# Optimization experiments

Hardware: AMD Instinct MI355X
Metric: run time of the kernel (lower is better)

Reference implementation:

```python
import jax, jax.numpy as jnp
import numpy as np

B, T = 64, 1024
RNN_DIM = 256          # lstm input/hidden dim
HID2 = 512             # 2*rnn_hidden_dim (bi-encoder output per char)
POS_DIM = 100
POS_SIZE = 48
LABEL = 96
POS_PAD = 0
APP_ID = 1


def setup_inputs() -> dict:
    key = jax.random.key(0)
    ks = jax.random.split(key, 9)
    s = 0.1
    enc = jax.random.normal(ks[0], (B, T, HID2), jnp.float32)
    pos_id = jax.random.randint(ks[1], (T, B), 0, POS_SIZE)
    start_index = jax.random.randint(ks[2], (T, B), 0, T)
    pos_table = (jax.random.normal(ks[3], (POS_SIZE, POS_DIM), jnp.float32) * s).at[POS_PAD].set(0.0)
    W_ih = jax.random.normal(ks[4], (4 * RNN_DIM, RNN_DIM), jnp.float32) * s
    b_ih = jnp.zeros((4 * RNN_DIM,), jnp.float32)
    W_hh = jax.random.normal(ks[5], (4 * RNN_DIM, RNN_DIM), jnp.float32) * s
    b_hh = jnp.zeros((4 * RNN_DIM,), jnp.float32)
    comb_W = jax.random.normal(ks[6], (RNN_DIM, HID2 + POS_DIM), jnp.float32) * s
    comb_b = jnp.zeros((RNN_DIM,), jnp.float32)
    lin_W = jax.random.normal(ks[7], (LABEL, HID2 + RNN_DIM), jnp.float32) * s
    return {"encoder_out": enc, "pos_table": pos_table, "W_ih": W_ih, "b_ih": b_ih,
            "W_hh": W_hh, "b_hh": b_hh, "comb_W": comb_W, "comb_b": comb_b,
            "lin_W": lin_W, "pos_id": pos_id, "start_index": start_index}


def reference(encoder_out, pos_table, W_ih, b_ih, W_hh, b_hh, comb_W, comb_b, lin_W,
              pos_id, start_index):
    Bn, Tn, D2 = encoder_out.shape
    H = W_hh.shape[1]
    L = lin_W.shape[0]
    dt = encoder_out.dtype
    # prefix sums: P[:, t] = sum of encoder_out[:, :t]  -> [B, T+1, D2]
    P = jnp.concatenate([jnp.zeros((Bn, 1, D2), dt), jnp.cumsum(encoder_out, axis=1)], axis=1)
    # step t consumes decisions made at step t-1 (state.pos_id[-1] / words_startindex[-1])
    prev_pos = jnp.concatenate([jnp.zeros((1, Bn), pos_id.dtype), pos_id[:-1]], axis=0)
    prev_start = jnp.concatenate([jnp.zeros((1, Bn), start_index.dtype), start_index[:-1]], axis=0)
    ts = jnp.arange(Tn)
    enc_t = jnp.swapaxes(encoder_out, 0, 1)   # [T, B, D2]
    P_t = jnp.swapaxes(P[:, :Tn], 0, 1)       # [T, B, D2]; P_t[t] = prefix up to t
    barange = jnp.arange(Bn)
    lab = jnp.arange(L)

    def step(carry, xs):
        h, c = carry
        t, pp, ps, Pt, et = xs
        # variable-length word avg-pool over chars [start, t)  (F.avg_pool1d)
        valid = (ps >= 0) & (t > 0)
        start = jnp.clip(jnp.minimum(ps, t - 1), 0, Tn - 1)
        wsum = Pt - P[barange, start]                       # [B, D2]
        length = jnp.maximum(t - start, 1).astype(dt)
        avg = jnp.where(valid[:, None], wsum / length[:, None], jnp.zeros((), dt))
        pe = pos_table[pp]                                  # [B, pos_dim]
        z = jnp.tanh(jnp.concatenate([pe, avg], axis=1) @ comb_W.T + comb_b)
        z = jnp.where(t > 0, z, jnp.zeros((), dt))          # t==0: z bucket of zeros
        # LSTMCell
        gates = z @ W_ih.T + b_ih + h @ W_hh.T + b_hh
        i_g, f_g, g_g, o_g = jnp.split(gates, 4, axis=1)
        c_new = jax.nn.sigmoid(f_g) * c + jax.nn.sigmoid(i_g) * jnp.tanh(g_g)
        h_new = jax.nn.sigmoid(o_g) * jnp.tanh(c_new)
        # output projection over [h_now, encoder_out[t]]
        out = jnp.concatenate([h_new, et], axis=1) @ lin_W.T
        out = jnp.where((t == 0) & (lab[None, :] == APP_ID), jnp.asarray(-1e10, dt), out)
        return (h_new, c_new), out

    h0 = jnp.zeros((Bn, H), dt)
    (_, _), outs = jax.lax.scan(step, (h0, h0), (ts, prev_pos, prev_start, P_t, enc_t))
    dec = jnp.swapaxes(outs, 0, 1).reshape(Bn * Tn, L)   # cat along dim 1 then view
    return jax.nn.log_softmax(dec, axis=1)
```

## Files before the change

kernel.cpp:

```cpp
#include <hip/hip_runtime.h>

typedef unsigned short u16;
typedef unsigned int u32;
typedef unsigned long long u64;
typedef __attribute__((ext_vector_type(8))) short short8;
typedef __attribute__((ext_vector_type(4))) float f32x4;
typedef __attribute__((ext_vector_type(8))) int i32x8;

#define B_ 64
#define T_ 1024
#define D2_ 512
#define HD_ 256
#define G4_ 1024
#define PD_ 100
#define KX_ 640
#define KO_ 768
#define LBL_ 96
#define LPAD_ 128
#define SCA 125
#define SCB 124

__device__ __forceinline__ float bf2f(u16 u) {
  u32 v = ((u32)u) << 16;
  return __builtin_bit_cast(float, v);
}
__device__ __forceinline__ u16 f2bf(float f) {
  u32 u = __builtin_bit_cast(u32, f);
  u32 r = (u + 0x7fffu + ((u >> 16) & 1u)) >> 16;
  return (u16)r;
}
__device__ __forceinline__ u32 pk2(float a, float b) {
  return (u32)f2bf(a) | ((u32)f2bf(b) << 16);
}
__device__ __forceinline__ float sgm(float x) {
  return __builtin_amdgcn_rcpf(1.f + __builtin_amdgcn_exp2f(-1.442695040888963f * x));
}
__device__ __forceinline__ float thh(float x) {
  return fmaf(-2.f,
              __builtin_amdgcn_rcpf(1.f + __builtin_amdgcn_exp2f(2.885390081777927f * x)),
              1.f);
}
__device__ __forceinline__ u32 enc4(float y) {
  float a = fabsf(y);
  u32 c = 0;
  c = a >= 0.25f ? 1u : c;
  c = a >= 0.75f ? 2u : c;
  c = a >= 1.25f ? 3u : c;
  c = a >= 1.75f ? 4u : c;
  c = a >= 2.5f ? 5u : c;
  c = a >= 3.5f ? 6u : c;
  c = a >= 5.0f ? 7u : c;
  return c | ((__builtin_bit_cast(u32, y) >> 28) & 8u);
}

__global__ __launch_bounds__(256) void k_prep(
    const float* combW, const float* Wih, const float* bih, const float* Whh,
    const float* bhh, const float* linW, u16* wc, u16* wih, u32* w4, u16* wlin,
    float* biasg) {
  int idx = blockIdx.x * 256 + threadIdx.x;
  if (idx < 256 * KX_) {
    int r = idx / KX_, c = idx % KX_;
    wc[idx] = f2bf(c < 612 ? combW[r * 612 + c] : 0.f);
    return;
  }
  idx -= 256 * KX_;
  if (idx < G4_ * HD_) { wih[idx] = f2bf(Wih[idx]); return; }
  idx -= G4_ * HD_;
  if (idx < G4_ * HD_ / 8) {
    int n = idx >> 5, c0 = (idx & 31) * 8;
    const float* wr = Whh + n * 256 + c0;
    u32 word = 0;
#pragma unroll
    for (int i = 0; i < 4; ++i) {
      u32 byte = enc4(wr[2 * i] * 8.f) | (enc4(wr[2 * i + 1] * 8.f) << 4);
      word |= byte << (8 * i);
    }
    w4[n * 32 + (c0 >> 3)] = word;
    return;
  }
  idx -= G4_ * HD_ / 8;
  if (idx < LPAD_ * KO_) {
    int r = idx / KO_;
    wlin[idx] = f2bf(r < LBL_ ? linW[idx] : 0.f);
    return;
  }
  idx -= LPAD_ * KO_;
  if (idx < G4_) biasg[idx] = bih[idx] + bhh[idx];
}

__global__ __launch_bounds__(512) void k_psum(const float* enc, float* S) {
  const int bc = blockIdx.x;
  const int d = threadIdx.x;
  const int b = bc >> 4, c = bc & 15;
  const float* e = enc + (((size_t)b * T_) + c * 64) * D2_ + d;
  float s = 0.f;
#pragma unroll 8
  for (int j = 0; j < 64; ++j) s += e[(size_t)j * D2_];
  S[(size_t)bc * D2_ + d] = s;
}

__global__ __launch_bounds__(512) void k_pwrite(const float* enc, const float* S,
                                                float* P) {
  const int bc = blockIdx.x;
  const int d = threadIdx.x;
  const int b = bc >> 4, c = bc & 15;
  float off = 0.f;
  for (int c2 = 0; c2 < c; ++c2) off += S[((size_t)(b * 16 + c2)) * D2_ + d];
  const float* e = enc + (((size_t)b * T_) + c * 64) * D2_ + d;
  float* p = P + (((size_t)b * T_) + c * 64) * D2_ + d;
#pragma unroll 4
  for (int j = 0; j < 64; ++j) {
    p[(size_t)j * D2_] = off;
    off += e[(size_t)j * D2_];
  }
}

__global__ __launch_bounds__(320) void k_xbuild(const float* P, const float* ptab,
                                                const int* pid, const int* sidx,
                                                u16* X) {
  const int tid = threadIdx.x;
  const int row = tid / 80;
  const int ir = tid - row * 80;
  const int m = blockIdx.x * 4 + row;
  const int t = m >> 6, b = m & 63;
  int pp = 0, ps = 0;
  if (t > 0) {
    pp = pid[(t - 1) * B_ + b];
    ps = sidx[(t - 1) * B_ + b];
  }
  bool valid = (ps >= 0) && (t > 0);
  int start = min(ps, t - 1);
  start = max(start, 0);
  start = min(start, T_ - 1);
  float invlen = 1.f / (float)max(t - start, 1);
  const float* Pt = P + ((size_t)b * T_ + t) * D2_;
  const float* Ps = P + ((size_t)b * T_ + start) * D2_;
  const int k0 = ir * 8;
  uint4 o;
  if (k0 >= 104 && k0 + 8 <= 612) {
    if (valid) {
      int d = k0 - 100;
      float4 t0 = *(const float4*)(Pt + d), t1 = *(const float4*)(Pt + d + 4);
      float4 s0 = *(const float4*)(Ps + d), s1 = *(const float4*)(Ps + d + 4);
      o.x = pk2((t0.x - s0.x) * invlen, (t0.y - s0.y) * invlen);
      o.y = pk2((t0.z - s0.z) * invlen, (t0.w - s0.w) * invlen);
      o.z = pk2((t1.x - s1.x) * invlen, (t1.y - s1.y) * invlen);
      o.w = pk2((t1.z - s1.z) * invlen, (t1.w - s1.w) * invlen);
    } else {
      o = (uint4){0, 0, 0, 0};
    }
  } else if (k0 + 8 <= 100) {
    const float* pr = ptab + pp * PD_ + k0;
    o.x = pk2(pr[0], pr[1]);
    o.y = pk2(pr[2], pr[3]);
    o.z = pk2(pr[4], pr[5]);
    o.w = pk2(pr[6], pr[7]);
  } else if (k0 >= 616) {
    o = (uint4){0, 0, 0, 0};
  } else {
    u32 ow[4];
#pragma unroll
    for (int j2 = 0; j2 < 4; ++j2) {
      float v[2];
#pragma unroll
      for (int jj = 0; jj < 2; ++jj) {
        int k = k0 + j2 * 2 + jj;
        float x;
        if (k < PD_) x = ptab[pp * PD_ + k];
        else if (k < 612) x = valid ? (Pt[k - PD_] - Ps[k - PD_]) * invlen : 0.f;
        else x = 0.f;
        v[jj] = x;
      }
      ow[j2] = pk2(v[0], v[1]);
    }
    o = (uint4){ow[0], ow[1], ow[2], ow[3]};
  }
  *(uint4*)(X + (size_t)m * KX_ + k0) = o;
}

template <int MODE>
__global__ __launch_bounds__(256, 2) void k_gemm(const u16* A, const u16* Bw,
                                                 const float* bias, u16* outb) {
  constexpr int K = (MODE == 0) ? KX_ : HD_;
  constexpr int NOUT = (MODE == 0) ? 256 : 1024;
  __shared__ u16 As[128][40];
  __shared__ u16 Bs[128][40];
  const int m0 = blockIdx.x * 128, n0 = blockIdx.y * 128;
  const int tid = threadIdx.x;
  const int w = tid >> 6, l = tid & 63;
  const int wr = w >> 1, wc = w & 1;
  const int l15 = l & 15, lh = l >> 4;
  const int srow = tid >> 2, sc8 = (tid & 3) * 8;
  int brow0, brow1;
  if constexpr (MODE == 1) {
    int j0 = n0 + srow, j1 = n0 + srow + 64;
    brow0 = (j0 & 3) * 256 + (j0 >> 2);
    brow1 = (j1 & 3) * 256 + (j1 >> 2);
  } else {
    brow0 = n0 + srow;
    brow1 = n0 + srow + 64;
  }
  f32x4 acc[4][4] = {};
  for (int k0 = 0; k0 < K; k0 += 32) {
    uint4 a0 = *(const uint4*)(A + (size_t)(m0 + srow) * K + k0 + sc8);
    uint4 a1 = *(const uint4*)(A + (size_t)(m0 + srow + 64) * K + k0 + sc8);
    uint4 b0 = *(const uint4*)(Bw + (size_t)brow0 * K + k0 + sc8);
    uint4 b1 = *(const uint4*)(Bw + (size_t)brow1 * K + k0 + sc8);
    __syncthreads();
    *(uint4*)&As[srow][sc8] = a0;
    *(uint4*)&As[srow + 64][sc8] = a1;
    *(uint4*)&Bs[srow][sc8] = b0;
    *(uint4*)&Bs[srow + 64][sc8] = b1;
    __syncthreads();
    short8 af[4], bf[4];
#pragma unroll
    for (int i = 0; i < 4; ++i) {
      af[i] = *(const short8*)&As[wr * 64 + i * 16 + l15][lh * 8];
      bf[i] = *(const short8*)&Bs[wc * 64 + i * 16 + l15][lh * 8];
    }
#pragma unroll
    for (int mi = 0; mi < 4; ++mi)
#pragma unroll
      for (int ni = 0; ni < 4; ++ni)
        acc[mi][ni] =
            __builtin_amdgcn_mfma_f32_16x16x32_bf16(af[mi], bf[ni], acc[mi][ni], 0, 0, 0);
  }
#pragma unroll
  for (int mi = 0; mi < 4; ++mi)
#pragma unroll
    for (int ni = 0; ni < 4; ++ni)
#pragma unroll
      for (int r = 0; r < 4; ++r) {
        int gm = m0 + wr * 64 + mi * 16 + lh * 4 + r;
        int gn = n0 + wc * 64 + ni * 16 + l15;
        float v = acc[mi][ni][r];
        if constexpr (MODE == 0) {
          v = tanhf(v + bias[gn]);
          if (gm < 64) v = 0.f;
          outb[(size_t)gm * NOUT + gn] = f2bf(v);
        } else {
          v += bias[(gn & 3) * 256 + (gn >> 2)];
          outb[(size_t)gm * NOUT + gn] = f2bf(v);
        }
      }
}

__global__ __launch_bounds__(512, 2) void k_seq(const u16* G, const u32* w4,
                                                u16* Hout) {
  __shared__ __align__(16) unsigned char hq[2][128];
  const int b = blockIdx.x;
  const int tid = threadIdx.x;
  const int w = tid >> 6, l = tid & 63;
  const int c16 = l & 15, quad = l >> 4;
  const unsigned char* w4b = (const unsigned char*)w4;
  uint4 Bf[2][4][2];
#pragma unroll
  for (int ct = 0; ct < 2; ++ct)
#pragma unroll
    for (int g = 0; g < 4; ++g) {
      int n = g * 256 + w * 32 + ct * 16 + c16;
#pragma unroll
      for (int kb = 0; kb < 2; ++kb)
        Bf[ct][g][kb] = *(const uint4*)(w4b + (size_t)n * 128 + kb * 64 + quad * 16);
    }
  if (tid < 128) hq[0][tid] = 0;
  const int myct = quad >> 1;
  const int mycell = w * 32 + myct * 16 + c16;
  const u16* gptr = G + (size_t)b * 1024 + mycell * 4;
  u64 gq = *(const u64*)gptr;
  float cc = 0.f;
  int cur = 0;
  __syncthreads();
  for (int t = 0; t < T_; ++t) {
    int tn = (t + 1 < T_) ? t + 1 : t;
    u64 ngq = *(const u64*)(gptr + (size_t)tn * 65536);
    uint4 a0 = *(const uint4*)&hq[cur][quad * 16];
    uint4 a1 = *(const uint4*)&hq[cur][64 + quad * 16];
    i32x8 A0 = (i32x8){(int)a0.x, (int)a0.y, (int)a0.z, (int)a0.w, 0, 0, 0, 0};
    i32x8 A1 = (i32x8){(int)a1.x, (int)a1.y, (int)a1.z, (int)a1.w, 0, 0, 0, 0};
    f32x4 acc[2][4];
#pragma unroll
    for (int ct = 0; ct < 2; ++ct)
#pragma unroll
      for (int g = 0; g < 4; ++g) {
        uint4 b0 = Bf[ct][g][0], b1 = Bf[ct][g][1];
        i32x8 B0 = (i32x8){(int)b0.x, (int)b0.y, (int)b0.z, (int)b0.w, 0, 0, 0, 0};
        i32x8 B1 = (i32x8){(int)b1.x, (int)b1.y, (int)b1.z, (int)b1.w, 0, 0, 0, 0};
        f32x4 z4 = (f32x4){0.f, 0.f, 0.f, 0.f};
        z4 = __builtin_amdgcn_mfma_scale_f32_16x16x128_f8f6f4(
            A0, B0, z4, 4, 4, 0, SCA, 0, SCB);
        z4 = __builtin_amdgcn_mfma_scale_f32_16x16x128_f8f6f4(
            A1, B1, z4, 4, 4, 0, SCA, 0, SCB);
        acc[ct][g] = z4;
      }
    bool hi = (myct != 0);
    float vi = (hi ? acc[1][0][0] : acc[0][0][0]) + bf2f((u16)gq);
    float vf = (hi ? acc[1][1][0] : acc[0][1][0]) + bf2f((u16)(gq >> 16));
    float vg = (hi ? acc[1][2][0] : acc[0][2][0]) + bf2f((u16)(gq >> 32));
    float vo = (hi ? acc[1][3][0] : acc[0][3][0]) + bf2f((u16)(gq >> 48));
    cc = sgm(vf) * cc + sgm(vi) * thh(vg);
    float h = sgm(vo) * thh(cc);
    u32 nib = enc4(h * 4.f);
    u32 nib2 = (u32)__shfl_xor((int)nib, 1);
    if ((quad & 1) == 0) {
      if ((c16 & 1) == 0)
        hq[cur ^ 1][mycell >> 1] = (unsigned char)(nib | (nib2 << 4));
      Hout[((size_t)b * 1024 + t) * 256 + mycell] = f2bf(h);
    }
    gq = ngq;
    cur ^= 1;
    __syncthreads();
  }
}

__global__ __launch_bounds__(256) void k_out(const u16* Hs, const float* enc,
                                             const u16* wlin, float* out) {
  __shared__ u16 As[64][40];
  __shared__ u16 Bs[128][40];
  const int m0 = blockIdx.x * 64;
  const int tid = threadIdx.x;
  const int srow = tid >> 2, sc8 = (tid & 3) * 8;
  const int brow = tid >> 1, bc16 = (tid & 1) * 16;
  const int w = tid >> 6, l = tid & 63;
  const int l15 = l & 15, lh = l >> 4;
  f32x4 acc[8] = {};
  for (int k0 = 0; k0 < KO_; k0 += 32) {
    int k = k0 + sc8;
    uint4 av;
    if (k < 256) {
      av = *(const uint4*)(Hs + (size_t)(m0 + srow) * 256 + k);
    } else {
      const float* src = enc + (size_t)(m0 + srow) * 512 + (k - 256);
      float4 f0 = *(const float4*)(src);
      float4 f1 = *(const float4*)(src + 4);
      av.x = pk2(f0.x, f0.y);
      av.y = pk2(f0.z, f0.w);
      av.z = pk2(f1.x, f1.y);
      av.w = pk2(f1.z, f1.w);
    }
    *(uint4*)&As[srow][sc8] = av;
    const u16* bsrc = wlin + (size_t)brow * KO_ + k0 + bc16;
    *(uint4*)&Bs[brow][bc16] = *(const uint4*)(bsrc);
    *(uint4*)&Bs[brow][bc16 + 8] = *(const uint4*)(bsrc + 8);
    __syncthreads();
    short8 a8 = *(const short8*)&As[16 * w + l15][lh * 8];
#pragma unroll
    for (int nt = 0; nt < 8; ++nt) {
      short8 b8 = *(const short8*)&Bs[nt * 16 + l15][lh * 8];
      acc[nt] = __builtin_amdgcn_mfma_f32_16x16x32_bf16(a8, b8, acc[nt], 0, 0, 0);
    }
    __syncthreads();
  }
#pragma unroll
  for (int r = 0; r < 4; ++r) {
    int gm = m0 + 16 * w + lh * 4 + r;
    float v[8];
#pragma unroll
    for (int nt = 0; nt < 8; ++nt) v[nt] = acc[nt][r];
    if ((gm & (T_ - 1)) == 0 && l15 == 1) v[0] = -1e10f;
    float mx = v[0];
#pragma unroll
    for (int nt = 1; nt < 6; ++nt) mx = fmaxf(mx, v[nt]);
#pragma unroll
    for (int s = 1; s < 16; s <<= 1) mx = fmaxf(mx, __shfl_xor(mx, s));
    float s0 = 0.f;
#pragma unroll
    for (int nt = 0; nt < 6; ++nt)
      s0 += __builtin_amdgcn_exp2f(1.442695040888963f * (v[nt] - mx));
#pragma unroll
    for (int s = 1; s < 16; s <<= 1) s0 += __shfl_xor(s0, s);
    float lg = __builtin_amdgcn_logf(s0) * 0.6931471805599453f + mx;
#pragma unroll
    for (int nt = 0; nt < 6; ++nt)
      out[(size_t)gm * LBL_ + nt * 16 + l15] = v[nt] - lg;
  }
}

extern "C" void kernel_launch(void* const* d_in, const int* in_sizes, int n_in,
                              void* d_out, int out_size, void* d_ws, size_t ws_size,
                              hipStream_t stream) {
  const float* enc = (const float*)d_in[0];
  const float* ptab = (const float*)d_in[1];
  const float* Wih = (const float*)d_in[2];
  const float* bih = (const float*)d_in[3];
  const float* Whh = (const float*)d_in[4];
  const float* bhh = (const float*)d_in[5];
  const float* combW = (const float*)d_in[6];
  const float* combb = (const float*)d_in[7];
  const float* linW = (const float*)d_in[8];
  const int* pid = (const int*)d_in[9];
  const int* sidx = (const int*)d_in[10];

  char* ws = (char*)d_ws;
  size_t off = 0;
  auto alloc = [&](size_t bytes) {
    void* p = ws + off;
    off += (bytes + 255) & ~(size_t)255;
    return p;
  };
  float* P = (float*)alloc((size_t)B_ * T_ * D2_ * 4);
  u16* Xb = (u16*)alloc((size_t)T_ * B_ * KX_ * 2);
  u16* Z = (u16*)alloc((size_t)T_ * B_ * HD_ * 2);
  u16* wc = (u16*)alloc(256 * KX_ * 2);
  u16* wih = (u16*)alloc(G4_ * HD_ * 2);
  u32* w4 = (u32*)alloc(G4_ * HD_ / 2);
  u16* wlin = (u16*)alloc(LPAD_ * KO_ * 2);
  float* biasg = (float*)alloc(G4_ * 4);
  u16* G = (u16*)P;
  u16* Hs = (u16*)Xb;
  float* S = (float*)Z;
  float* out = (float*)d_out;

  k_prep<<<2180, 256, 0, stream>>>(combW, Wih, bih, Whh, bhh, linW, wc, wih, w4,
                                   wlin, biasg);
  k_psum<<<B_ * 16, 512, 0, stream>>>(enc, S);
  k_pwrite<<<B_ * 16, 512, 0, stream>>>(enc, S, P);
  k_xbuild<<<T_ * B_ / 4, 320, 0, stream>>>(P, ptab, pid, sidx, Xb);
  dim3 g3(512, 2);
  k_gemm<0><<<g3, 256, 0, stream>>>(Xb, wc, combb, Z);
  dim3 g4(512, 8);
  k_gemm<1><<<g4, 256, 0, stream>>>(Z, wih, biasg, G);
  k_seq<<<B_, 512, 0, stream>>>(G, w4, Hs);
  k_out<<<1024, 256, 0, stream>>>(Hs, enc, wlin, out);
}
```

Before: 906.1 us.

## Store prefix sums as bf16 and swap GEMM grid axes for tile reuse

The prefix-sum buffer P is now written in bf16 instead of fp32, which halves the bytes k_pwrite writes and k_xbuild reads. The reduced precision of large prefix sums can hurt the accuracy of the word averages, since it takes the difference of two nearby large values. Separately, both GEMM launches swap their grid axes so that consecutive blocks share the same A row-tile across N tiles, which should improve cache reuse of A. The workspace region is resized to hold the gate buffer G and is aliased with the bf16 P.

```diff
diff --git a/kernel.cpp b/kernel.cpp
--- a/kernel.cpp
+++ b/kernel.cpp
@@ -100,22 +100,22 @@
 }
 
 __global__ __launch_bounds__(512) void k_pwrite(const float* enc, const float* S,
-                                                float* P) {
+                                                u16* Pb) {
   const int bc = blockIdx.x;
   const int d = threadIdx.x;
   const int b = bc >> 4, c = bc & 15;
   float off = 0.f;
   for (int c2 = 0; c2 < c; ++c2) off += S[((size_t)(b * 16 + c2)) * D2_ + d];
   const float* e = enc + (((size_t)b * T_) + c * 64) * D2_ + d;
-  float* p = P + (((size_t)b * T_) + c * 64) * D2_ + d;
+  u16* p = Pb + (((size_t)b * T_) + c * 64) * D2_ + d;
 #pragma unroll 4
   for (int j = 0; j < 64; ++j) {
-    p[(size_t)j * D2_] = off;
+    p[(size_t)j * D2_] = f2bf(off);
     off += e[(size_t)j * D2_];
   }
 }
 
-__global__ __launch_bounds__(320) void k_xbuild(const float* P, const float* ptab,
+__global__ __launch_bounds__(320) void k_xbuild(const u16* Pb, const float* ptab,
                                                 const int* pid, const int* sidx,
                                                 u16* X) {
   const int tid = threadIdx.x;
@@ -133,19 +133,25 @@
   start = max(start, 0);
   start = min(start, T_ - 1);
   float invlen = 1.f / (float)max(t - start, 1);
-  const float* Pt = P + ((size_t)b * T_ + t) * D2_;
-  const float* Ps = P + ((size_t)b * T_ + start) * D2_;
+  const u16* Pt = Pb + ((size_t)b * T_ + t) * D2_;
+  const u16* Ps = Pb + ((size_t)b * T_ + start) * D2_;
   const int k0 = ir * 8;
   uint4 o;
   if (k0 >= 104 && k0 + 8 <= 612) {
     if (valid) {
       int d = k0 - 100;
-      float4 t0 = *(const float4*)(Pt + d), t1 = *(const float4*)(Pt + d + 4);
-      float4 s0 = *(const float4*)(Ps + d), s1 = *(const float4*)(Ps + d + 4);
-      o.x = pk2((t0.x - s0.x) * invlen, (t0.y - s0.y) * invlen);
-      o.y = pk2((t0.z - s0.z) * invlen, (t0.w - s0.w) * invlen);
-      o.z = pk2((t1.x - s1.x) * invlen, (t1.y - s1.y) * invlen);
-      o.w = pk2((t1.z - s1.z) * invlen, (t1.w - s1.w) * invlen);
+      ushort4 ta = *(const ushort4*)(Pt + d);
+      ushort4 tb = *(const ushort4*)(Pt + d + 4);
+      ushort4 sa = *(const ushort4*)(Ps + d);
+      ushort4 sb = *(const ushort4*)(Ps + d + 4);
+      o.x = pk2((bf2f(ta.x) - bf2f(sa.x)) * invlen,
+                (bf2f(ta.y) - bf2f(sa.y)) * invlen);
+      o.y = pk2((bf2f(ta.z) - bf2f(sa.z)) * invlen,
+                (bf2f(ta.w) - bf2f(sa.w)) * invlen);
+      o.z = pk2((bf2f(tb.x) - bf2f(sb.x)) * invlen,
+                (bf2f(tb.y) - bf2f(sb.y)) * invlen);
+      o.w = pk2((bf2f(tb.z) - bf2f(sb.z)) * invlen,
+                (bf2f(tb.w) - bf2f(sb.w)) * invlen);
     } else {
       o = (uint4){0, 0, 0, 0};
     }
@@ -167,7 +173,8 @@
         int k = k0 + j2 * 2 + jj;
         float x;
         if (k < PD_) x = ptab[pp * PD_ + k];
-        else if (k < 612) x = valid ? (Pt[k - PD_] - Ps[k - PD_]) * invlen : 0.f;
+        else if (k < 612)
+          x = valid ? (bf2f(Pt[k - PD_]) - bf2f(Ps[k - PD_])) * invlen : 0.f;
         else x = 0.f;
         v[jj] = x;
       }
@@ -185,7 +192,7 @@
   constexpr int NOUT = (MODE == 0) ? 256 : 1024;
   __shared__ u16 As[128][40];
   __shared__ u16 Bs[128][40];
-  const int m0 = blockIdx.x * 128, n0 = blockIdx.y * 128;
+  const int m0 = blockIdx.y * 128, n0 = blockIdx.x * 128;
   const int tid = threadIdx.x;
   const int w = tid >> 6, l = tid & 63;
   const int wr = w >> 1, wc = w & 1;
@@ -398,7 +405,7 @@
     off += (bytes + 255) & ~(size_t)255;
     return p;
   };
-  float* P = (float*)alloc((size_t)B_ * T_ * D2_ * 4);
+  void* reg1 = alloc((size_t)B_ * T_ * G4_ * 2);
   u16* Xb = (u16*)alloc((size_t)T_ * B_ * KX_ * 2);
   u16* Z = (u16*)alloc((size_t)T_ * B_ * HD_ * 2);
   u16* wc = (u16*)alloc(256 * KX_ * 2);
@@ -406,7 +413,8 @@
   u32* w4 = (u32*)alloc(G4_ * HD_ / 2);
   u16* wlin = (u16*)alloc(LPAD_ * KO_ * 2);
   float* biasg = (float*)alloc(G4_ * 4);
-  u16* G = (u16*)P;
+  u16* Pb = (u16*)reg1;
+  u16* G = (u16*)reg1;
   u16* Hs = (u16*)Xb;
   float* S = (float*)Z;
   float* out = (float*)d_out;
@@ -414,11 +422,11 @@
   k_prep<<<2180, 256, 0, stream>>>(combW, Wih, bih, Whh, bhh, linW, wc, wih, w4,
                                    wlin, biasg);
   k_psum<<<B_ * 16, 512, 0, stream>>>(enc, S);
-  k_pwrite<<<B_ * 16, 512, 0, stream>>>(enc, S, P);
-  k_xbuild<<<T_ * B_ / 4, 320, 0, stream>>>(P, ptab, pid, sidx, Xb);
-  dim3 g3(512, 2);
+  k_pwrite<<<B_ * 16, 512, 0, stream>>>(enc, S, Pb);
+  k_xbuild<<<T_ * B_ / 4, 320, 0, stream>>>(Pb, ptab, pid, sidx, Xb);
+  dim3 g3(2, 512);
   k_gemm<0><<<g3, 256, 0, stream>>>(Xb, wc, combb, Z);
-  dim3 g4(512, 8);
+  dim3 g4(8, 512);
   k_gemm<1><<<g4, 256, 0, stream>>>(Z, wih, biasg, G);
   k_seq<<<B_, 512, 0, stream>>>(G, w4, Hs);
   k_out<<<1024, 256, 0, stream>>>(Hs, enc, wlin, out);
```

New measurement: 870.6 us, median of 2. 3.9% less time.
